# Performance work log

Hardware: AMD Instinct MI355X
Metric: run time of the kernel (lower is better)

Reference implementation:

```python
import jax, jax.numpy as jnp
import numpy as np
import math

BS, S, E, H, DK = 32, 512, 512, 8, 64


def setup_inputs() -> dict:
    key = jax.random.key(0)
    ks = jax.random.split(key, 10)
    q = jax.random.normal(ks[0], (BS, S, E), jnp.float32)
    k = jax.random.normal(ks[1], (BS, S, E), jnp.float32)
    v = jax.random.normal(ks[2], (BS, S, E), jnp.float32)
    # strictly-causal mask: allowed where col < row (np.triu(k=0)==0)
    mask = jnp.tril(jnp.ones((S, S), bool), -1)[None, None]
    sc = 1.0 / math.sqrt(E)  # xavier-ish scale for square linears
    Wq = jax.random.normal(ks[3], (E, E), jnp.float32) * sc
    Wk = jax.random.normal(ks[4], (E, E), jnp.float32) * sc
    Wv = jax.random.normal(ks[5], (E, E), jnp.float32) * sc
    Wo = jax.random.normal(ks[6], (E, E), jnp.float32) * sc
    bq = jnp.zeros((E,), jnp.float32)
    bk = jnp.zeros((E,), jnp.float32)
    bv = jnp.zeros((E,), jnp.float32)
    bo = jnp.zeros((E,), jnp.float32)
    gammas = jax.random.normal(ks[7], (H, 1, 1), jnp.float32) * 0.5
    return {"q": q, "k": k, "v": v, "mask": mask, "zero_pad": 1,
            "Wq": Wq, "bq": bq, "Wk": Wk, "bk": bk, "Wv": Wv, "bv": bv,
            "Wo": Wo, "bo": bo, "gammas": gammas}


def reference(q, k, v, mask, zero_pad, Wq, bq, Wk, bk, Wv, bv, Wo, bo, gammas):
    bs = q.shape[0]
    # projections (torch Linear: x @ W.T + b), split heads -> [b,h,s,d]
    def heads(x, W, b):
        return (x @ W.T + b).reshape(bs, S, H, DK).transpose(0, 2, 1, 3)
    qh, kh, vh = heads(q, Wq, bq), heads(k, Wk, bk), heads(v, Wv, bv)

    scores = jnp.einsum('bhqd,bhkd->bhqk', qh, kh) / math.sqrt(DK)

    # --- distance-decay term (no-grad in original) ---
    neg = jnp.float32(-1e32)
    scores_ = jnp.where(mask, scores, neg)
    scores_ = jax.nn.softmax(scores_, axis=-1) * mask.astype(scores.dtype)
    distcum = jnp.cumsum(scores_, axis=-1)
    disttotal = jnp.sum(scores_, axis=-1, keepdims=True)
    idx = jnp.arange(S)
    position_effect = jnp.abs(idx[None, :] - idx[:, None]).astype(scores.dtype)[None, None]
    dist_scores = jnp.sqrt(jnp.clip((disttotal - distcum) * position_effect, 0.0))
    dist_scores = jax.lax.stop_gradient(dist_scores)

    gamma = -jax.nn.softplus(gammas)[None]  # [1,h,1,1]
    total_effect = jnp.clip(jnp.exp(dist_scores * gamma), 1e-5, 1e5)

    scores = scores * total_effect
    scores = jnp.where(mask, scores, neg)
    scores = jax.nn.softmax(scores, axis=-1)
    if zero_pad:
        scores = scores.at[:, :, 0, :].set(0.0)

    out = jnp.einsum('bhqk,bhkd->bhqd', scores, vh)
    concat = out.transpose(0, 2, 1, 3).reshape(bs, S, E)
    return concat @ Wo.T + bo
```

## Files before the change

kernel.cpp:

```cpp
#include <hip/hip_runtime.h>
#include <hip/hip_bf16.h>
#include <hip/hip_fp16.h>
#include <stdint.h>

#define BSZ 32
#define SEQ 512
#define EMB 512
#define NH  8
#define DKD 64
#define LOG2E 1.4426950408889634f

typedef float f32x4 __attribute__((ext_vector_type(4)));
typedef short s16x8 __attribute__((ext_vector_type(8)));

#if __has_builtin(__builtin_amdgcn_exp2f)
#define EXP2(x) __builtin_amdgcn_exp2f(x)
#else
#define EXP2(x) exp2f(x)
#endif
#define RCP(x) __builtin_amdgcn_rcpf(x)

__device__ inline unsigned short f2bf(float f) {
  union { float f; unsigned u; } v; v.f = f;
  unsigned r = v.u + 0x7fffu + ((v.u >> 16) & 1u);
  return (unsigned short)(r >> 16);
}

__device__ inline ushort4 pack4bf(float4 v) {
  union { __hip_bfloat162 h2[2]; ushort4 u4; } cv;
  cv.h2[0] = __float22bfloat162_rn(make_float2(v.x, v.y));
  cv.h2[1] = __float22bfloat162_rn(make_float2(v.z, v.w));
  return cv.u4;
}

__device__ inline void stage16(const void* g, void* l) {
#if defined(__has_builtin) && __has_builtin(__builtin_amdgcn_global_load_lds)
  __builtin_amdgcn_global_load_lds(
      (const __attribute__((address_space(1))) void*)g,
      (__attribute__((address_space(3))) void*)l, 16, 0, 0);
#else
  *reinterpret_cast<uint4*>(l) = *reinterpret_cast<const uint4*>(g);
#endif
}

template<int CTRL>
__device__ inline float dpp_shr_f(float x) {
  return __builtin_bit_cast(float,
    __builtin_amdgcn_update_dpp(0, __builtin_bit_cast(int, x), CTRL, 0xf, 0xf, true));
}
__device__ inline float rlane(float v, int l) {
  return __builtin_bit_cast(float, __builtin_amdgcn_readlane(__builtin_bit_cast(int, v), l));
}

__global__ __launch_bounds__(256)
void wcvt(const float* __restrict__ w0, const float* __restrict__ w1,
          const float* __restrict__ w2, const float* __restrict__ w3,
          unsigned short* __restrict__ o0, unsigned short* __restrict__ o1,
          unsigned short* __restrict__ o2, unsigned short* __restrict__ o3)
{
  const float* src = (blockIdx.y == 0) ? w0 : (blockIdx.y == 1) ? w1
                   : (blockIdx.y == 2) ? w2 : w3;
  unsigned short* dst = (blockIdx.y == 0) ? o0 : (blockIdx.y == 1) ? o1
                      : (blockIdx.y == 2) ? o2 : o3;
  const int i = (blockIdx.x * 256 + threadIdx.x) * 8;
  float4 a = *reinterpret_cast<const float4*>(src + i);
  float4 b = *reinterpret_cast<const float4*>(src + i + 4);
  union { ushort4 p[2]; s16x8 v; } cc;
  cc.p[0] = pack4bf(a); cc.p[1] = pack4bf(b);
  *reinterpret_cast<s16x8*>(dst + i) = cc.v;
}

template<int MODE>
__global__ __launch_bounds__(256)
void gemm_bt(const void* __restrict__ Av, const unsigned short* __restrict__ Bw,
             const float* __restrict__ bias, void* __restrict__ C,
             int M, int N, int K, float oscale)
{
  constexpr int ASZ = (MODE == 3) ? 8192 : 16384;
  __shared__ __align__(16) char smem[ASZ + 8192];
  char* const sA = smem;
  char* const sB = smem + ASZ;
  const int tid  = threadIdx.x;
  const int lane = tid & 63;
  const int w    = tid >> 6;
  const int m0   = blockIdx.y * 128;
  const int n0   = blockIdx.x * 128;
  const int wr   = (w >> 1) * 64;
  const int wc   = (w & 1) * 64;
  const int base = w * 1024 + lane * 16;

  f32x4 acc[4][4] = {};

  for (int k0 = 0; k0 < K; k0 += 32) {
    if constexpr (MODE != 3) {
      const float* A = (const float*)Av;
      #pragma unroll
      for (int c = 0; c < 4; ++c) {
        const int flat = c * 4096 + base;
        const int row  = flat >> 7;
        const int gl   = ((flat >> 4) & 7) ^ (row & 7);
        stage16(&A[(size_t)(m0 + row) * K + k0 + gl * 4], sA + flat);
      }
    } else {
      const unsigned short* A = (const unsigned short*)Av;
      #pragma unroll
      for (int c = 0; c < 2; ++c) {
        const int flat = c * 4096 + base;
        const int r    = flat >> 7;
        const int gl   = ((flat >> 4) & 7) ^ (r & 7);
        const int row  = r + ((gl >> 2) << 6);
        stage16(&A[(size_t)(m0 + row) * K + k0 + (gl & 3) * 8], sA + flat);
      }
    }
    #pragma unroll
    for (int c = 0; c < 2; ++c) {
      const int flat = c * 4096 + base;
      const int r    = flat >> 7;
      const int gl   = ((flat >> 4) & 7) ^ (r & 7);
      const int nn   = r + ((gl >> 2) << 6);
      stage16(&Bw[(size_t)(n0 + nn) * K + k0 + (gl & 3) * 8], sB + flat);
    }
    __syncthreads();

    s16x8 af[4], bf[4];
    #pragma unroll
    for (int i = 0; i < 4; ++i) {
      const int row = wr + i * 16 + (lane & 15);
      if constexpr (MODE != 3) {
        const int g1 = (lane >> 4) << 1;
        float4 v1 = *reinterpret_cast<const float4*>(sA + row * 128 + ((g1 ^ (row & 7)) << 4));
        float4 v2 = *reinterpret_cast<const float4*>(sA + row * 128 + (((g1 + 1) ^ (row & 7)) << 4));
        union { ushort4 p[2]; s16x8 v; } cc;
        cc.p[0] = pack4bf(v1); cc.p[1] = pack4bf(v2);
        af[i] = cc.v;
      } else {
        const int r  = row & 63;
        const int gl = ((row >> 6) << 2) + (lane >> 4);
        af[i] = *reinterpret_cast<const s16x8*>(sA + r * 128 + ((gl ^ (r & 7)) << 4));
      }
    }
    #pragma unroll
    for (int j = 0; j < 4; ++j) {
      const int n  = wc + j * 16 + (lane & 15);
      const int r  = n & 63;
      const int gl = ((n >> 6) << 2) + (lane >> 4);
      bf[j] = *reinterpret_cast<const s16x8*>(sB + r * 128 + ((gl ^ (r & 7)) << 4));
    }
    #pragma unroll
    for (int i = 0; i < 4; ++i)
      #pragma unroll
      for (int j = 0; j < 4; ++j)
        acc[i][j] = __builtin_amdgcn_mfma_f32_16x16x32_bf16(af[i], bf[j], acc[i][j], 0, 0, 0);
    __syncthreads();
  }

  #pragma unroll
  for (int i = 0; i < 4; ++i)
    #pragma unroll
    for (int j = 0; j < 4; ++j)
      #pragma unroll
      for (int r = 0; r < 4; ++r) {
        const int gm = m0 + wr + i * 16 + (lane >> 4) * 4 + r;
        const int gn = n0 + wc + j * 16 + (lane & 15);
        const float vv = (acc[i][j][r] + bias[gn]) * oscale;
        if (MODE == 3) {
          ((float*)C)[(size_t)gm * N + gn] = vv;
        } else {
          const int b = gm >> 9, s = gm & 511, h = gn >> 6, d = gn & 63;
          const size_t off = (MODE == 0)
              ? ((size_t)(b * NH + h) * SEQ + s) * DKD + d
              : ((size_t)(b * NH + h) * DKD + d) * SEQ + s;
          ((unsigned short*)C)[off] = f2bf(vv);
        }
      }
}

template<int R>
__device__ inline void phase2_rows(unsigned short* s_lds, int w, int lane,
                                   int q0, int zp, float g2)
{
  constexpr int L  = 64 / R;
  constexpr int IT = 4 / R;
  const int seg = lane / L;
  const int li  = lane & (L - 1);
  const int jb  = li * 8;
  const float NEGINF = -__builtin_inff();
  #pragma unroll
  for (int it = 0; it < IT; ++it) {
    const int r  = w * 4 + it * R + seg;
    const int qg = q0 + r;
    const int gs = li ^ (r & 7);
    unsigned short* rowp = &s_lds[r * 512 + gs * 8];
    float pn2[8];
    if (qg == 0) {
      const float u = zp ? 0.0f : (1.0f / 512.0f);
      #pragma unroll
      for (int i = 0; i < 8; ++i) pn2[i] = u;
    } else {
      float sL[8];
      {
        s16x8 raw = *reinterpret_cast<const s16x8*>(rowp);
        union { s16x8 v; __half2 h[4]; } u; u.v = raw;
        #pragma unroll
        for (int i = 0; i < 4; ++i) {
          float2 f = __half22float2(u.h[i]);
          sL[2 * i] = f.x; sL[2 * i + 1] = f.y;
        }
      }
      #pragma unroll
      for (int i = 0; i < 8; ++i) sL[i] = (jb + i < qg) ? sL[i] : NEGINF;
      float p[8], c[8];
      float run = 0.f;
      #pragma unroll
      for (int i = 0; i < 8; ++i) { p[i] = EXP2(sL[i]); run += p[i]; c[i] = run; }
      float t = run;
      t += dpp_shr_f<0x111>(t);
      t += dpp_shr_f<0x112>(t);
      t += dpp_shr_f<0x114>(t);
      t += dpp_shr_f<0x118>(t);
      float tot;
      if constexpr (R == 1) {
        const float r0 = rlane(t, 15), r1 = rlane(t, 31), r2 = rlane(t, 47);
        const float a1 = r0, a2 = r0 + r1, a3 = a2 + r2;
        tot = a3 + rlane(t, 63);
        t += (lane >= 48) ? a3 : (lane >= 32) ? a2 : (lane >= 16) ? a1 : 0.f;
      } else if constexpr (R == 2) {
        const float r0 = rlane(t, 15), r2 = rlane(t, 47);
        t += (lane & 16) ? ((lane < 32) ? r0 : r2) : 0.f;
        tot = __shfl(t, lane | 31, 64);
      } else {
        tot = __shfl(t, lane | 15, 64);
      }
      const float pre  = tot - (t - run);
      const float g2r  = g2 * __builtin_amdgcn_sqrtf(RCP(tot));
      const float fb   = (float)(qg - jb);
      float p2[8]; float run2 = 0.f;
      #pragma unroll
      for (int i = 0; i < 8; ++i) {
        const float rem = pre - c[i];
        const float arg = fmaxf(rem * (fb - (float)i), 0.f);
        float te = EXP2(__builtin_amdgcn_sqrtf(arg) * g2r);
        te = fmaxf(te, 1e-5f);
        p2[i] = EXP2(sL[i] * te);
        run2 += p2[i];
      }
      float y = run2;
      y += dpp_shr_f<0x111>(y);
      y += dpp_shr_f<0x112>(y);
      y += dpp_shr_f<0x114>(y);
      y += dpp_shr_f<0x118>(y);
      float s2;
      if constexpr (R == 1) {
        s2 = rlane(y, 15) + rlane(y, 31) + rlane(y, 47) + rlane(y, 63);
      } else if constexpr (R == 2) {
        y += (lane & 16) ? ((lane < 32) ? rlane(y, 15) : rlane(y, 47)) : 0.f;
        s2 = __shfl(y, lane | 31, 64);
      } else {
        s2 = __shfl(y, lane | 15, 64);
      }
      const float inv2 = RCP(s2);
      #pragma unroll
      for (int i = 0; i < 8; ++i) pn2[i] = p2[i] * inv2;
    }
    union { __hip_bfloat162 h2[4]; uint4 u; } pk;
    pk.h2[0] = __float22bfloat162_rn(make_float2(pn2[0], pn2[1]));
    pk.h2[1] = __float22bfloat162_rn(make_float2(pn2[2], pn2[3]));
    pk.h2[2] = __float22bfloat162_rn(make_float2(pn2[4], pn2[5]));
    pk.h2[3] = __float22bfloat162_rn(make_float2(pn2[6], pn2[7]));
    *reinterpret_cast<uint4*>(rowp) = pk.u;
  }
}

__global__ __launch_bounds__(256)
void attn_kernel(const unsigned short* __restrict__ Qh,
                 const unsigned short* __restrict__ Kh,
                 const unsigned short* __restrict__ Vt,
                 unsigned short* __restrict__ Aout,
                 const float* __restrict__ gammas,
                 const int* __restrict__ zero_pad)
{
  __shared__ __align__(16) unsigned short s_lds[16 * 512];
  const int tid = threadIdx.x, lane = tid & 63, w = tid >> 6;
  const int lin = blockIdx.x;
  const int x   = lin & 7;
  const int u   = lin >> 3;
  const int qb  = u >> 5;
  const int h   = u & 7;
  const int b   = x * 4 + ((u >> 3) & 3);
  const int q0  = qb * 16;
  const size_t bh = (size_t)b * NH + h;
  const unsigned short* Qp = Qh + bh * SEQ * DKD;
  const unsigned short* Kp = Kh + bh * SEQ * DKD;
  const unsigned short* Vp = Vt + bh * DKD * SEQ;
  const int zp = zero_pad[0];
  const float g2 = -log1pf(__expf(gammas[h])) * LOG2E;

  s16x8 aq[2];
  #pragma unroll
  for (int kt = 0; kt < 2; ++kt)
    aq[kt] = *reinterpret_cast<const s16x8*>(&Qp[(q0 + (lane & 15)) * DKD + kt * 32 + (lane >> 4) * 8]);
  {
    const int frag = (lane >> 4) * 8;
    auto loadK = [&](int t, s16x8* kb) {
      const int n = t * 16 + (lane & 15);
      kb[0] = *reinterpret_cast<const s16x8*>(&Kp[n * DKD + frag]);
      kb[1] = *reinterpret_cast<const s16x8*>(&Kp[n * DKD + 32 + frag]);
    };
    auto tilecomp = [&](int t, const s16x8* kb) {
      f32x4 acc = {};
      acc = __builtin_amdgcn_mfma_f32_16x16x32_bf16(aq[0], kb[0], acc, 0, 0, 0);
      acc = __builtin_amdgcn_mfma_f32_16x16x32_bf16(aq[1], kb[1], acc, 0, 0, 0);
      const int n = t * 16 + (lane & 15);
      #pragma unroll
      for (int r = 0; r < 4; ++r) {
        const int row = (lane >> 4) * 4 + r;
        const int idx = row * 512 + ((((n >> 3) ^ (row & 7)) << 3) + (n & 7));
        s_lds[idx] = __half_as_ushort(__float2half(acc[r]));
      }
    };
    int t = w;
    if (t <= qb) {
      s16x8 cur[2], nxt[2];
      loadK(t, cur);
      while (true) {
        const int tn = t + 4;
        if (tn <= qb) {
          loadK(tn, nxt);
          tilecomp(t, cur);
          cur[0] = nxt[0]; cur[1] = nxt[1];
          t = tn;
        } else {
          tilecomp(t, cur);
          break;
        }
      }
    }
  }
  __syncthreads();

  if (zp == 0 && qb == 0) {
    phase2_rows<1>(s_lds, w, lane, q0, zp, g2);
  } else if (qb < 8) {
    phase2_rows<4>(s_lds, w, lane, q0, zp, g2);
  } else if (qb < 16) {
    phase2_rows<2>(s_lds, w, lane, q0, zp, g2);
  } else {
    phase2_rows<1>(s_lds, w, lane, q0, zp, g2);
  }
  __syncthreads();

  f32x4 oacc = {};
  const int row  = lane & 15;
  const int koff = lane >> 4;
  const int rsw  = row & 7;
  const unsigned short* vbase = &Vp[(w * 16 + row) * SEQ + koff * 8];
  const int ks_end = (qb == 0 && zp == 0) ? 16 : (qb >> 1) + 1;
  int ks0 = 0;
  for (; ks0 + 4 <= ks_end; ks0 += 4) {
    s16x8 vb[4], pa[4];
    #pragma unroll
    for (int uu = 0; uu < 4; ++uu) {
      const int ks = ks0 + uu;
      vb[uu] = *reinterpret_cast<const s16x8*>(&vbase[ks * 32]);
      pa[uu] = *reinterpret_cast<const s16x8*>(&s_lds[row * 512 + ((ks * 4 + koff) ^ rsw) * 8]);
    }
    #pragma unroll
    for (int uu = 0; uu < 4; ++uu)
      oacc = __builtin_amdgcn_mfma_f32_16x16x32_bf16(pa[uu], vb[uu], oacc, 0, 0, 0);
  }
  for (; ks0 < ks_end; ++ks0) {
    s16x8 vb = *reinterpret_cast<const s16x8*>(&vbase[ks0 * 32]);
    s16x8 pa = *reinterpret_cast<const s16x8*>(&s_lds[row * 512 + ((ks0 * 4 + koff) ^ rsw) * 8]);
    oacc = __builtin_amdgcn_mfma_f32_16x16x32_bf16(pa, vb, oacc, 0, 0, 0);
  }
  #pragma unroll
  for (int r = 0; r < 4; ++r) {
    const int orow = (lane >> 4) * 4 + r;
    const int ocol = w * 16 + (lane & 15);
    Aout[((size_t)b * SEQ + (q0 + orow)) * EMB + h * DKD + ocol] = f2bf(oacc[r]);
  }
}

extern "C" void kernel_launch(void* const* d_in, const int* in_sizes, int n_in,
                              void* d_out, int out_size, void* d_ws, size_t ws_size,
                              hipStream_t stream)
{
  const float* q  = (const float*)d_in[0];
  const float* k  = (const float*)d_in[1];
  const float* v  = (const float*)d_in[2];
  const int*   zp = (const int*)d_in[4];
  const float* Wq = (const float*)d_in[5];
  const float* bq = (const float*)d_in[6];
  const float* Wk = (const float*)d_in[7];
  const float* bk = (const float*)d_in[8];
  const float* Wv = (const float*)d_in[9];
  const float* bv = (const float*)d_in[10];
  const float* Wo = (const float*)d_in[11];
  const float* bo = (const float*)d_in[12];
  const float* gm = (const float*)d_in[13];

  char* ws = (char*)d_ws;
  const size_t HB = (size_t)BSZ * NH * SEQ * DKD * sizeof(unsigned short);
  const size_t WB = (size_t)EMB * EMB * sizeof(unsigned short);
  unsigned short* Qh  = (unsigned short*)(ws);
  unsigned short* Kh  = (unsigned short*)(ws + HB);
  unsigned short* Vt  = (unsigned short*)(ws + 2 * HB);
  unsigned short* At  = (unsigned short*)(ws + 3 * HB);
  unsigned short* Wqb = (unsigned short*)(ws + 4 * HB);
  unsigned short* Wkb = (unsigned short*)(ws + 4 * HB + WB);
  unsigned short* Wvb = (unsigned short*)(ws + 4 * HB + 2 * WB);
  unsigned short* Wob = (unsigned short*)(ws + 4 * HB + 3 * WB);

  const int M = BSZ * SEQ, N = EMB, K = EMB;
  dim3 ggrid(N / 128, M / 128);
  wcvt<<<dim3(128, 4), 256, 0, stream>>>(Wq, Wk, Wv, Wo, Wqb, Wkb, Wvb, Wob);
  gemm_bt<0><<<ggrid, 256, 0, stream>>>(q, Wqb, bq, Qh, M, N, K, 0.125f * LOG2E);
  gemm_bt<0><<<ggrid, 256, 0, stream>>>(k, Wkb, bk, Kh, M, N, K, 1.0f);
  gemm_bt<1><<<ggrid, 256, 0, stream>>>(v, Wvb, bv, Vt, M, N, K, 1.0f);
  attn_kernel<<<8192, 256, 0, stream>>>(Qh, Kh, Vt, At, gm, zp);
  gemm_bt<3><<<ggrid, 256, 0, stream>>>(At, Wob, bo, d_out, M, N, K, 1.0f);
}
```

Baseline: 170.5 us.

## Fuse Q/K/V projection GEMMs into one launch with double-buffered LDS staging

Merges the three projection GEMMs into a single kernel launch of 1536 blocks, with the block index remapped so that blocks sharing an A row tile land on the same XCD for L2 reuse. Both the projection and output GEMMs now double-buffer their LDS tiles, issuing the next k-slice's loads before computing the current one, which removes one barrier per iteration. This is meant to cut launch gaps and expose memory latency overlap. In exchange, the projection kernel uses twice the LDS (48KB), which may lower occupancy.

After: 177.8 us. 1.04x slower.

```diff
diff --git a/kernel.cpp b/kernel.cpp
--- a/kernel.cpp
+++ b/kernel.cpp
@@ -70,47 +70,47 @@
   *reinterpret_cast<s16x8*>(dst + i) = cc.v;
 }
 
-template<int MODE>
 __global__ __launch_bounds__(256)
-void gemm_bt(const void* __restrict__ Av, const unsigned short* __restrict__ Bw,
-             const float* __restrict__ bias, void* __restrict__ C,
-             int M, int N, int K, float oscale)
+void proj_gemm(const float* __restrict__ q, const float* __restrict__ k,
+               const float* __restrict__ v,
+               const unsigned short* __restrict__ Wq,
+               const unsigned short* __restrict__ Wk,
+               const unsigned short* __restrict__ Wv,
+               const float* __restrict__ bq, const float* __restrict__ bk,
+               const float* __restrict__ bv,
+               unsigned short* __restrict__ Qh, unsigned short* __restrict__ Kh,
+               unsigned short* __restrict__ Vt, float qscale)
 {
-  constexpr int ASZ = (MODE == 3) ? 8192 : 16384;
-  __shared__ __align__(16) char smem[ASZ + 8192];
-  char* const sA = smem;
-  char* const sB = smem + ASZ;
+  __shared__ __align__(16) char smem[2 * 24576];
   const int tid  = threadIdx.x;
   const int lane = tid & 63;
   const int w    = tid >> 6;
-  const int m0   = blockIdx.y * 128;
-  const int n0   = blockIdx.x * 128;
+  const int lin  = blockIdx.x;
+  const int x    = lin & 7;
+  const int j    = lin >> 3;
+  const int P    = x * 48 + (j >> 2);
+  const int proj = P >> 7;
+  const int m0   = (P & 127) * 128;
+  const int n0   = (j & 3) * 128;
+  const float* A = (proj == 0) ? q : (proj == 1) ? k : v;
+  const unsigned short* Bw = (proj == 0) ? Wq : (proj == 1) ? Wk : Wv;
+  const float* bias = (proj == 0) ? bq : (proj == 1) ? bk : bv;
+  const float oscale = (proj == 0) ? qscale : 1.0f;
+  const int K = EMB;
+
   const int wr   = (w >> 1) * 64;
   const int wc   = (w & 1) * 64;
   const int base = w * 1024 + lane * 16;
 
-  f32x4 acc[4][4] = {};
-
-  for (int k0 = 0; k0 < K; k0 += 32) {
-    if constexpr (MODE != 3) {
-      const float* A = (const float*)Av;
-      #pragma unroll
-      for (int c = 0; c < 4; ++c) {
-        const int flat = c * 4096 + base;
-        const int row  = flat >> 7;
-        const int gl   = ((flat >> 4) & 7) ^ (row & 7);
-        stage16(&A[(size_t)(m0 + row) * K + k0 + gl * 4], sA + flat);
-      }
-    } else {
-      const unsigned short* A = (const unsigned short*)Av;
-      #pragma unroll
-      for (int c = 0; c < 2; ++c) {
-        const int flat = c * 4096 + base;
-        const int r    = flat >> 7;
-        const int gl   = ((flat >> 4) & 7) ^ (r & 7);
-        const int row  = r + ((gl >> 2) << 6);
-        stage16(&A[(size_t)(m0 + row) * K + k0 + (gl & 3) * 8], sA + flat);
-      }
+  auto stage = [&](int buf, int k0) {
+    char* sA = smem + buf * 24576;
+    char* sB = sA + 16384;
+    #pragma unroll
+    for (int c = 0; c < 4; ++c) {
+      const int flat = c * 4096 + base;
+      const int row  = flat >> 7;
+      const int gl   = ((flat >> 4) & 7) ^ (row & 7);
+      stage16(&A[(size_t)(m0 + row) * K + k0 + gl * 4], sA + flat);
     }
     #pragma unroll
     for (int c = 0; c < 2; ++c) {
@@ -120,58 +120,155 @@
       const int nn   = r + ((gl >> 2) << 6);
       stage16(&Bw[(size_t)(n0 + nn) * K + k0 + (gl & 3) * 8], sB + flat);
     }
-    __syncthreads();
-
+  };
+
+  f32x4 acc[4][4] = {};
+  auto compute = [&](int buf) {
+    char* sA = smem + buf * 24576;
+    char* sB = sA + 16384;
     s16x8 af[4], bf[4];
     #pragma unroll
     for (int i = 0; i < 4; ++i) {
       const int row = wr + i * 16 + (lane & 15);
-      if constexpr (MODE != 3) {
-        const int g1 = (lane >> 4) << 1;
-        float4 v1 = *reinterpret_cast<const float4*>(sA + row * 128 + ((g1 ^ (row & 7)) << 4));
-        float4 v2 = *reinterpret_cast<const float4*>(sA + row * 128 + (((g1 + 1) ^ (row & 7)) << 4));
-        union { ushort4 p[2]; s16x8 v; } cc;
-        cc.p[0] = pack4bf(v1); cc.p[1] = pack4bf(v2);
-        af[i] = cc.v;
-      } else {
-        const int r  = row & 63;
-        const int gl = ((row >> 6) << 2) + (lane >> 4);
-        af[i] = *reinterpret_cast<const s16x8*>(sA + r * 128 + ((gl ^ (r & 7)) << 4));
-      }
-    }
-    #pragma unroll
-    for (int j = 0; j < 4; ++j) {
-      const int n  = wc + j * 16 + (lane & 15);
+      const int g1  = (lane >> 4) << 1;
+      float4 v1 = *reinterpret_cast<const float4*>(sA + row * 128 + ((g1 ^ (row & 7)) << 4));
+      float4 v2 = *reinterpret_cast<const float4*>(sA + row * 128 + (((g1 + 1) ^ (row & 7)) << 4));
+      union { ushort4 p[2]; s16x8 vv; } cc;
+      cc.p[0] = pack4bf(v1); cc.p[1] = pack4bf(v2);
+      af[i] = cc.vv;
+    }
+    #pragma unroll
+    for (int jj = 0; jj < 4; ++jj) {
+      const int n  = wc + jj * 16 + (lane & 15);
       const int r  = n & 63;
       const int gl = ((n >> 6) << 2) + (lane >> 4);
-      bf[j] = *reinterpret_cast<const s16x8*>(sB + r * 128 + ((gl ^ (r & 7)) << 4));
+      bf[jj] = *reinterpret_cast<const s16x8*>(sB + r * 128 + ((gl ^ (r & 7)) << 4));
     }
     #pragma unroll
     for (int i = 0; i < 4; ++i)
       #pragma unroll
-      for (int j = 0; j < 4; ++j)
-        acc[i][j] = __builtin_amdgcn_mfma_f32_16x16x32_bf16(af[i], bf[j], acc[i][j], 0, 0, 0);
+      for (int jj = 0; jj < 4; ++jj)
+        acc[i][jj] = __builtin_amdgcn_mfma_f32_16x16x32_bf16(af[i], bf[jj], acc[i][jj], 0, 0, 0);
+  };
+
+  stage(0, 0);
+  __syncthreads();
+  int cur = 0;
+  for (int t = 0; t < 15; ++t) {
+    stage(cur ^ 1, (t + 1) * 32);
+    compute(cur);
     __syncthreads();
-  }
+    cur ^= 1;
+  }
+  compute(cur);
 
   #pragma unroll
   for (int i = 0; i < 4; ++i)
     #pragma unroll
-    for (int j = 0; j < 4; ++j)
+    for (int jj = 0; jj < 4; ++jj)
       #pragma unroll
       for (int r = 0; r < 4; ++r) {
         const int gm = m0 + wr + i * 16 + (lane >> 4) * 4 + r;
-        const int gn = n0 + wc + j * 16 + (lane & 15);
-        const float vv = (acc[i][j][r] + bias[gn]) * oscale;
-        if (MODE == 3) {
-          ((float*)C)[(size_t)gm * N + gn] = vv;
-        } else {
-          const int b = gm >> 9, s = gm & 511, h = gn >> 6, d = gn & 63;
-          const size_t off = (MODE == 0)
-              ? ((size_t)(b * NH + h) * SEQ + s) * DKD + d
-              : ((size_t)(b * NH + h) * DKD + d) * SEQ + s;
-          ((unsigned short*)C)[off] = f2bf(vv);
-        }
+        const int gn = n0 + wc + jj * 16 + (lane & 15);
+        const float vv = (acc[i][jj][r] + bias[gn]) * oscale;
+        const int b = gm >> 9, s = gm & 511, h = gn >> 6, d = gn & 63;
+        if (proj == 2)
+          Vt[((size_t)(b * NH + h) * DKD + d) * SEQ + s] = f2bf(vv);
+        else if (proj == 1)
+          Kh[((size_t)(b * NH + h) * SEQ + s) * DKD + d] = f2bf(vv);
+        else
+          Qh[((size_t)(b * NH + h) * SEQ + s) * DKD + d] = f2bf(vv);
+      }
+}
+
+__global__ __launch_bounds__(256)
+void out_gemm(const unsigned short* __restrict__ At,
+              const unsigned short* __restrict__ Wo,
+              const float* __restrict__ bo, float* __restrict__ C)
+{
+  __shared__ __align__(16) char smem[2 * 16384];
+  const int tid  = threadIdx.x;
+  const int lane = tid & 63;
+  const int w    = tid >> 6;
+  const int lin  = blockIdx.x;
+  const int x    = lin & 7;
+  const int j    = lin >> 3;
+  const int P    = x * 16 + (j >> 2);
+  const int m0   = P * 128;
+  const int n0   = (j & 3) * 128;
+  const int K = EMB, N = EMB;
+
+  const int wr   = (w >> 1) * 64;
+  const int wc   = (w & 1) * 64;
+  const int base = w * 1024 + lane * 16;
+
+  auto stage = [&](int buf, int k0) {
+    char* sA = smem + buf * 16384;
+    char* sB = sA + 8192;
+    #pragma unroll
+    for (int c = 0; c < 2; ++c) {
+      const int flat = c * 4096 + base;
+      const int r    = flat >> 7;
+      const int gl   = ((flat >> 4) & 7) ^ (r & 7);
+      const int row  = r + ((gl >> 2) << 6);
+      stage16(&At[(size_t)(m0 + row) * K + k0 + (gl & 3) * 8], sA + flat);
+    }
+    #pragma unroll
+    for (int c = 0; c < 2; ++c) {
+      const int flat = c * 4096 + base;
+      const int r    = flat >> 7;
+      const int gl   = ((flat >> 4) & 7) ^ (r & 7);
+      const int nn   = r + ((gl >> 2) << 6);
+      stage16(&Wo[(size_t)(n0 + nn) * K + k0 + (gl & 3) * 8], sB + flat);
+    }
+  };
+
+  f32x4 acc[4][4] = {};
+  auto compute = [&](int buf) {
+    char* sA = smem + buf * 16384;
+    char* sB = sA + 8192;
+    s16x8 af[4], bf[4];
+    #pragma unroll
+    for (int i = 0; i < 4; ++i) {
+      const int row = wr + i * 16 + (lane & 15);
+      const int r   = row & 63;
+      const int gl  = ((row >> 6) << 2) + (lane >> 4);
+      af[i] = *reinterpret_cast<const s16x8*>(sA + r * 128 + ((gl ^ (r & 7)) << 4));
+    }
+    #pragma unroll
+    for (int jj = 0; jj < 4; ++jj) {
+      const int n  = wc + jj * 16 + (lane & 15);
+      const int r  = n & 63;
+      const int gl = ((n >> 6) << 2) + (lane >> 4);
+      bf[jj] = *reinterpret_cast<const s16x8*>(sB + r * 128 + ((gl ^ (r & 7)) << 4));
+    }
+    #pragma unroll
+    for (int i = 0; i < 4; ++i)
+      #pragma unroll
+      for (int jj = 0; jj < 4; ++jj)
+        acc[i][jj] = __builtin_amdgcn_mfma_f32_16x16x32_bf16(af[i], bf[jj], acc[i][jj], 0, 0, 0);
+  };
+
+  stage(0, 0);
+  __syncthreads();
+  int cur = 0;
+  for (int t = 0; t < 15; ++t) {
+    stage(cur ^ 1, (t + 1) * 32);
+    compute(cur);
+    __syncthreads();
+    cur ^= 1;
+  }
+  compute(cur);
+
+  #pragma unroll
+  for (int i = 0; i < 4; ++i)
+    #pragma unroll
+    for (int jj = 0; jj < 4; ++jj)
+      #pragma unroll
+      for (int r = 0; r < 4; ++r) {
+        const int gm = m0 + wr + i * 16 + (lane >> 4) * 4 + r;
+        const int gn = n0 + wc + jj * 16 + (lane & 15);
+        C[(size_t)gm * N + gn] = acc[i][jj][r] + bo[gn];
       }
 }
 
@@ -411,12 +508,9 @@
   unsigned short* Wvb = (unsigned short*)(ws + 4 * HB + 2 * WB);
   unsigned short* Wob = (unsigned short*)(ws + 4 * HB + 3 * WB);
 
-  const int M = BSZ * SEQ, N = EMB, K = EMB;
-  dim3 ggrid(N / 128, M / 128);
   wcvt<<<dim3(128, 4), 256, 0, stream>>>(Wq, Wk, Wv, Wo, Wqb, Wkb, Wvb, Wob);
-  gemm_bt<0><<<ggrid, 256, 0, stream>>>(q, Wqb, bq, Qh, M, N, K, 0.125f * LOG2E);
-  gemm_bt<0><<<ggrid, 256, 0, stream>>>(k, Wkb, bk, Kh, M, N, K, 1.0f);
-  gemm_bt<1><<<ggrid, 256, 0, stream>>>(v, Wvb, bv, Vt, M, N, K, 1.0f);
+  proj_gemm<<<1536, 256, 0, stream>>>(q, k, v, Wqb, Wkb, Wvb, bq, bk, bv,
+                                      Qh, Kh, Vt, 0.125f * LOG2E);
   attn_kernel<<<8192, 256, 0, stream>>>(Qh, Kh, Vt, At, gm, zp);
-  gemm_bt<3><<<ggrid, 256, 0, stream>>>(At, Wob, bo, d_out, M, N, K, 1.0f);
-}
+  out_gemm<<<512, 256, 0, stream>>>(At, Wob, bo, (float*)d_out);
+}
```
